# Kernel optimization log

Measured on AMD Instinct MI355X. Metric: run time of the kernel, lower is better.

The kernel has to match this reference:

```python
import jax, jax.numpy as jnp
import numpy as np

HEADS = 8
EPS = 1e-5


def setup_inputs() -> dict:
    key = jax.random.key(0)
    ks = jax.random.split(key, 4)
    B, S, N, C = 1, 192, 256, 256
    msa = jax.random.normal(ks[0], (B, S, N, C), dtype=jnp.float32)
    w_qkv = jax.random.normal(ks[1], (3 * C, C), dtype=jnp.float32) * 0.02
    b_qkv = jnp.zeros((3 * C,), dtype=jnp.float32)
    w_out = jax.random.normal(ks[2], (C, C), dtype=jnp.float32) * 0.02
    b_out = jnp.zeros((C,), dtype=jnp.float32)
    gamma = jnp.ones((C,), dtype=jnp.float32)
    beta = jnp.zeros((C,), dtype=jnp.float32)
    return {"msa": msa, "w_qkv": w_qkv, "b_qkv": b_qkv, "w_out": w_out,
            "b_out": b_out, "gamma": gamma, "beta": beta}


def reference(msa, w_qkv, b_qkv, w_out, b_out, gamma, beta):
    B, S, N, C = msa.shape
    H = HEADS
    D = C // H
    scale = D ** -0.5
    # column attention: attend over the S (MSA depth) axis per residue n
    msa_t = jnp.transpose(msa, (0, 2, 1, 3))                 # [B,N,S,C]
    qkv = msa_t @ w_qkv.T + b_qkv                             # [B,N,S,3C]
    qkv = qkv.reshape(B, N, S, 3, H, D)
    q, k, v = qkv[..., 0, :, :], qkv[..., 1, :, :], qkv[..., 2, :, :]  # [B,N,S,H,D]
    attn = jnp.einsum('bnshd,bnthd->bnhst', q, k) * scale     # [B,N,H,S,S]
    attn = jax.nn.softmax(attn, axis=-1)
    out = jnp.einsum('bnhst,bnthd->bnshd', attn, v).reshape(B, N, S, C)
    out = jnp.transpose(out, (0, 2, 1, 3))                    # [B,S,N,C]
    out = out @ w_out.T + b_out
    x = msa + out
    mu = jnp.mean(x, axis=-1, keepdims=True)
    var = jnp.mean(jnp.square(x - mu), axis=-1, keepdims=True)
    return (x - mu) * jax.lax.rsqrt(var + EPS) * gamma + beta
```

## Files before the change

### kernel.cpp

```cpp
#include <hip/hip_runtime.h>
#include <stdint.h>

#define S_DIM 192
#define N_DIM 256
#define C_DIM 256
#define H_DIM 8
#define D_DIM 32
#define TOK   (N_DIM * S_DIM)
#define QKV_STRIDE (N_DIM * H_DIM * S_DIM * D_DIM)

typedef float f32x4 __attribute__((ext_vector_type(4)));
typedef float f32x16 __attribute__((ext_vector_type(16)));
typedef short bf16x8 __attribute__((ext_vector_type(8)));

__device__ __forceinline__ unsigned short f2bf(float f) {
  union { float f; unsigned u; } v; v.f = f;
  unsigned r = v.u + 0x7FFFu + ((v.u >> 16) & 1u);
  return (unsigned short)(r >> 16);
}

__device__ __forceinline__ unsigned cvt_pk_bf16(float lo, float hi) {
  unsigned r;
  asm("v_cvt_pk_bf16_f32 %0, %1, %2" : "=v"(r) : "v"(lo), "v"(hi));
  return r;
}

__device__ __forceinline__ void gl2lds16(const void* g, void* l) {
  __builtin_amdgcn_global_load_lds(
      (const __attribute__((address_space(1))) unsigned int*)g,
      (__attribute__((address_space(3))) unsigned int*)l, 16, 0, 0);
}

__global__ __launch_bounds__(256) void k_prep(const float* __restrict__ msa,
                                              unsigned short* __restrict__ A,
                                              const float* __restrict__ wq,
                                              const float* __restrict__ wo,
                                              unsigned short* __restrict__ dq,
                                              unsigned short* __restrict__ do_) {
  int b = blockIdx.x;
  if (b < 12288) {
    int tid = b * 256 + threadIdx.x;
    int token = tid >> 6;
    int c4 = tid & 63;
    int n = token / S_DIM;
    int s = token - n * S_DIM;
    float4 v = *(const float4*)(msa + ((size_t)(s * N_DIM + n) << 8) + (c4 << 2));
    ushort4 o;
    o.x = f2bf(v.x); o.y = f2bf(v.y); o.z = f2bf(v.z); o.w = f2bf(v.w);
    *(ushort4*)(A + ((size_t)token << 8) + (c4 << 2)) = o;
  } else {
    int tid = (b - 12288) * 256 + threadIdx.x;
    const float* src; unsigned short* dst; int idx;
    if (tid < 49152) { src = wq; dst = dq; idx = tid; }
    else { src = wo; dst = do_; idx = tid - 49152; }
    float4 v = *(const float4*)(src + (size_t)idx * 4);
    ushort4 o;
    o.x = f2bf(v.x); o.y = f2bf(v.y); o.z = f2bf(v.z); o.w = f2bf(v.w);
    *(ushort4*)(dst + (size_t)idx * 4) = o;
  }
}

__global__ __launch_bounds__(256) void k_qkv(const unsigned short* __restrict__ A,
                                             const unsigned short* __restrict__ W,
                                             const float* __restrict__ bq,
                                             unsigned short* __restrict__ qkv) {
  __shared__ unsigned short As[128 * 64];
  __shared__ unsigned short Bs[128 * 64];
  const int tid = threadIdx.x;
  const int lane = tid & 63, wid = tid >> 6;
  const int l16 = lane & 15, lg = lane >> 4;
  const int wr = wid >> 1, wc = wid & 1;
  const int bm0 = blockIdx.x * 128;
  const int bn0 = blockIdx.y * 128;
  const int lrow = lane >> 3, lchunk = lane & 7;
  const int sw = ((lchunk ^ lrow) * 8);

  f32x4 acc[4][4] = {};

  for (int ks = 0; ks < 4; ks++) {
    const int k0 = ks * 64;
    __syncthreads();
#pragma unroll
    for (int q = 0; q < 4; q++) {
      int base_row = wid * 32 + q * 8;
      gl2lds16(A + (size_t)(bm0 + base_row + lrow) * 256 + k0 + sw, &As[base_row * 64]);
    }
#pragma unroll
    for (int q = 0; q < 4; q++) {
      int base_row = wid * 32 + q * 8;
      gl2lds16(W + (size_t)(bn0 + base_row + lrow) * 256 + k0 + sw, &Bs[base_row * 64]);
    }
    __syncthreads();
#pragma unroll
    for (int kk = 0; kk < 2; kk++) {
      const int xr = ((kk * 4 + lg) ^ (l16 & 7)) * 8;
      bf16x8 a[4], b[4];
#pragma unroll
      for (int m = 0; m < 4; m++)
        a[m] = *(const bf16x8*)&As[(wr * 64 + m * 16 + l16) * 64 + xr];
#pragma unroll
      for (int n2 = 0; n2 < 4; n2++)
        b[n2] = *(const bf16x8*)&Bs[(wc * 64 + n2 * 16 + l16) * 64 + xr];
      if (bn0 < 512) {
#pragma unroll
        for (int m = 0; m < 4; m++)
#pragma unroll
          for (int n2 = 0; n2 < 4; n2++)
            acc[m][n2] = __builtin_amdgcn_mfma_f32_16x16x32_bf16(b[n2], a[m], acc[m][n2], 0, 0, 0);
      } else {
#pragma unroll
        for (int m = 0; m < 4; m++)
#pragma unroll
          for (int n2 = 0; n2 < 4; n2++)
            acc[m][n2] = __builtin_amdgcn_mfma_f32_16x16x32_bf16(a[m], b[n2], acc[m][n2], 0, 0, 0);
      }
    }
  }

  const int t3 = bn0 >> 8;
  if (t3 < 2) {
#pragma unroll
    for (int n2 = 0; n2 < 4; n2++) {
      int j0 = bn0 + wc * 64 + n2 * 16 + lg * 4;
      float4 b4 = *(const float4*)&bq[j0];
      int c0 = j0 & 255;
      int h = c0 >> 5, d0 = c0 & 31;
#pragma unroll
      for (int m = 0; m < 4; m++) {
        int token = bm0 + wr * 64 + m * 16 + l16;
        int n = token / S_DIM;
        int s = token - n * S_DIM;
        ushort4 o;
        o.x = f2bf(acc[m][n2][0] + b4.x);
        o.y = f2bf(acc[m][n2][1] + b4.y);
        o.z = f2bf(acc[m][n2][2] + b4.z);
        o.w = f2bf(acc[m][n2][3] + b4.w);
        *(ushort4*)(qkv + (size_t)t3 * QKV_STRIDE +
                    ((size_t)((n * 8 + h) * 192 + s)) * 32 + d0) = o;
      }
    }
  } else {
#pragma unroll
    for (int n2 = 0; n2 < 4; n2++) {
      int j = bn0 + wc * 64 + n2 * 16 + l16;
      int hd = j - 512;
      int h = hd >> 5, d = hd & 31;
      float bias = bq[j];
#pragma unroll
      for (int m = 0; m < 4; m++) {
        int t0 = bm0 + wr * 64 + m * 16 + lg * 4;
        int n = t0 / S_DIM;
        int s0 = t0 - n * S_DIM;
        ushort4 o;
        o.x = f2bf(acc[m][n2][0] + bias);
        o.y = f2bf(acc[m][n2][1] + bias);
        o.z = f2bf(acc[m][n2][2] + bias);
        o.w = f2bf(acc[m][n2][3] + bias);
        *(ushort4*)(qkv + (size_t)2 * QKV_STRIDE + ((size_t)(n * 8 + h) * 32 + d) * 192 + s0) = o;
      }
    }
  }
}

__global__ __launch_bounds__(384) void k_attn2(const unsigned short* __restrict__ qkv,
                                               unsigned short* __restrict__ attn_out) {
  const int lane = threadIdx.x & 63;
  const int l32 = lane & 31;
  const int hi = lane >> 5;
  const int qt = threadIdx.x >> 6;
  const int nh = blockIdx.x;
  const int n = nh >> 3, h = nh & 7;
  const unsigned short* Qp = qkv + (size_t)nh * (192 * 32);
  const unsigned short* Kp = qkv + (size_t)QKV_STRIDE + (size_t)nh * (192 * 32);
  const unsigned short* Vt = qkv + (size_t)2 * QKV_STRIDE + (size_t)nh * (32 * 192);
  const int q0 = qt * 32;

  bf16x8 bq0 = *(const bf16x8*)(Qp + (q0 + l32) * 32 + hi * 8);
  bf16x8 bq1 = *(const bf16x8*)(Qp + (q0 + l32) * 32 + 16 + hi * 8);

  f32x16 accO = {};
  float m_run = -1e30f, l_run = 0.f;
  const float scale = 0.17677669529663687f;
  const float DEFER = 8.0f / 0.17677669529663687f;

  bf16x8 ka0 = *(const bf16x8*)(Kp + l32 * 32 + hi * 8);
  bf16x8 ka1 = *(const bf16x8*)(Kp + l32 * 32 + 16 + hi * 8);

  for (int t = 0; t < 6; t++) {
    bf16x8 kn0, kn1;
    if (t < 5) {
      kn0 = *(const bf16x8*)(Kp + ((t + 1) * 32 + l32) * 32 + hi * 8);
      kn1 = *(const bf16x8*)(Kp + ((t + 1) * 32 + l32) * 32 + 16 + hi * 8);
    }
    f32x16 sv = {};
    sv = __builtin_amdgcn_mfma_f32_32x32x16_bf16(ka0, bq0, sv, 0, 0, 0);
    sv = __builtin_amdgcn_mfma_f32_32x32x16_bf16(ka1, bq1, sv, 0, 0, 0);

    bf16x8 bv0 = *(const bf16x8*)(Vt + (size_t)l32 * 192 + t * 32 + hi * 8);
    bf16x8 bv1 = *(const bf16x8*)(Vt + (size_t)l32 * 192 + t * 32 + 16 + hi * 8);

    float tmx = sv[0];
#pragma unroll
    for (int r = 1; r < 16; r++) tmx = fmaxf(tmx, sv[r]);
    tmx = fmaxf(tmx, __shfl_xor(tmx, 32));

    bool need = tmx > m_run + DEFER;
    if (__ballot(need)) {
      float m_new = fmaxf(m_run, tmx);
      float corr = __expf((m_run - m_new) * scale);
      l_run *= corr;
#pragma unroll
      for (int r = 0; r < 16; r++) {
        int qr = (r & 3) + 8 * (r >> 2) + 4 * hi;
        accO[r] *= __shfl(corr, qr);
      }
      m_run = m_new;
    }

    float ssum = 0.f;
#pragma unroll
    for (int r = 0; r < 16; r++) {
      float p = __expf((sv[r] - m_run) * scale);
      sv[r] = p;
      ssum += p;
    }
    ssum += __shfl_xor(ssum, 32);
    l_run += ssum;

    unsigned pk[8];
#pragma unroll
    for (int g = 0; g < 4; g++) {
      pk[2 * g]     = cvt_pk_bf16(sv[4 * g],     sv[4 * g + 1]);
      pk[2 * g + 1] = cvt_pk_bf16(sv[4 * g + 2], sv[4 * g + 3]);
    }

#pragma unroll
    for (int kh = 0; kh < 2; kh++) {
      unsigned sa = hi ? pk[4 * kh]     : pk[4 * kh + 2];
      unsigned sb = hi ? pk[4 * kh + 1] : pk[4 * kh + 3];
      unsigned pa = __shfl_xor((int)sa, 32);
      unsigned pb = __shfl_xor((int)sb, 32);
      union { unsigned u[4]; bf16x8 v; } af;
      af.u[0] = hi ? pa : pk[4 * kh];
      af.u[1] = hi ? pb : pk[4 * kh + 1];
      af.u[2] = hi ? pk[4 * kh + 2] : pa;
      af.u[3] = hi ? pk[4 * kh + 3] : pb;
      accO = __builtin_amdgcn_mfma_f32_32x32x16_bf16(af.v, kh ? bv1 : bv0, accO, 0, 0, 0);
    }
    ka0 = kn0; ka1 = kn1;
  }

  float inv = 1.0f / l_run;
#pragma unroll
  for (int r = 0; r < 16; r++) {
    int qr = (r & 3) + 8 * (r >> 2) + 4 * hi;
    float v = accO[r] * __shfl(inv, qr);
    attn_out[((size_t)((q0 + qr) * 256 + n)) * 256 + h * 32 + l32] = f2bf(v);
  }
}

__global__ __launch_bounds__(256) void k_out(const unsigned short* __restrict__ Aat,
                                             const unsigned short* __restrict__ W,
                                             const float* __restrict__ bo,
                                             const float* __restrict__ msa,
                                             const float* __restrict__ gamma,
                                             const float* __restrict__ beta,
                                             float* __restrict__ out) {
  __shared__ unsigned short As[128 * 64];
  __shared__ unsigned short Bs[256 * 64];
  const int tid = threadIdx.x;
  const int lane = tid & 63, wid = tid >> 6;
  const int l16 = lane & 15, lg = lane >> 4;
  const int bm0 = blockIdx.x * 128;
  const int lrow = lane >> 3, lchunk = lane & 7;
  const int sw = ((lchunk ^ lrow) * 8);

  f32x4 acc[2][16] = {};

  for (int ks = 0; ks < 4; ks++) {
    const int k0 = ks * 64;
    __syncthreads();
#pragma unroll
    for (int q = 0; q < 4; q++) {
      int base_row = wid * 32 + q * 8;
      gl2lds16(Aat + (size_t)(bm0 + base_row + lrow) * 256 + k0 + sw, &As[base_row * 64]);
    }
#pragma unroll
    for (int q = 0; q < 8; q++) {
      int base_row = wid * 64 + q * 8;
      gl2lds16(W + (size_t)(base_row + lrow) * 256 + k0 + sw, &Bs[base_row * 64]);
    }
    __syncthreads();
#pragma unroll
    for (int kk = 0; kk < 2; kk++) {
      const int xr = ((kk * 4 + lg) ^ (l16 & 7)) * 8;
      bf16x8 a[2];
#pragma unroll
      for (int m = 0; m < 2; m++)
        a[m] = *(const bf16x8*)&As[(wid * 32 + m * 16 + l16) * 64 + xr];
#pragma unroll
      for (int c = 0; c < 16; c++) {
        bf16x8 b = *(const bf16x8*)&Bs[(c * 16 + l16) * 64 + xr];
#pragma unroll
        for (int m = 0; m < 2; m++)
          acc[m][c] = __builtin_amdgcn_mfma_f32_16x16x32_bf16(a[m], b, acc[m][c], 0, 0, 0);
      }
    }
  }

#pragma unroll
  for (int m = 0; m < 2; m++) {
#pragma unroll
    for (int c = 0; c < 16; c++) {
      int col = c * 16 + l16;
      float bias = bo[col];
#pragma unroll
      for (int i = 0; i < 4; i++) {
        int row = bm0 + wid * 32 + m * 16 + lg * 4 + i;
        acc[m][c][i] += bias + msa[(size_t)row * 256 + col];
      }
    }
#pragma unroll
    for (int i = 0; i < 4; i++) {
      float s1 = 0.f, s2 = 0.f;
#pragma unroll
      for (int c = 0; c < 16; c++) { float x = acc[m][c][i]; s1 += x; s2 += x * x; }
      s1 += __shfl_xor(s1, 1); s2 += __shfl_xor(s2, 1);
      s1 += __shfl_xor(s1, 2); s2 += __shfl_xor(s2, 2);
      s1 += __shfl_xor(s1, 4); s2 += __shfl_xor(s2, 4);
      s1 += __shfl_xor(s1, 8); s2 += __shfl_xor(s2, 8);
      float mu = s1 * (1.0f / 256.0f);
      float var = s2 * (1.0f / 256.0f) - mu * mu;
      float rstd = rsqrtf(var + 1e-5f);
      int row = bm0 + wid * 32 + m * 16 + lg * 4 + i;
#pragma unroll
      for (int c = 0; c < 16; c++) {
        int col = c * 16 + l16;
        float y = (acc[m][c][i] - mu) * rstd * gamma[col] + beta[col];
        out[(size_t)row * 256 + col] = y;
      }
    }
  }
}

extern "C" void kernel_launch(void* const* d_in, const int* in_sizes, int n_in,
                              void* d_out, int out_size, void* d_ws, size_t ws_size,
                              hipStream_t stream) {
  const float* msa   = (const float*)d_in[0];
  const float* w_qkv = (const float*)d_in[1];
  const float* b_qkv = (const float*)d_in[2];
  const float* w_out = (const float*)d_in[3];
  const float* b_out = (const float*)d_in[4];
  const float* gamma = (const float*)d_in[5];
  const float* beta  = (const float*)d_in[6];
  float* out = (float*)d_out;

  char* ws = (char*)d_ws;
  unsigned short* A      = (unsigned short*)(ws);
  unsigned short* qkvbuf = (unsigned short*)(ws + 25165824ull);
  unsigned short* wq_bf  = (unsigned short*)(ws + 4ull * 25165824ull);
  unsigned short* wo_bf  = (unsigned short*)(ws + 4ull * 25165824ull + 393216ull);

  k_prep<<<12544, 256, 0, stream>>>(msa, A, w_qkv, w_out, wq_bf, wo_bf);
  dim3 g2(384, 6);
  k_qkv<<<g2, 256, 0, stream>>>(A, wq_bf, b_qkv, qkvbuf);
  k_attn2<<<2048, 384, 0, stream>>>(qkvbuf, A);
  k_out<<<384, 256, 0, stream>>>(A, wo_bf, b_out, msa, gamma, beta, out);
}
```

Measured before the change: 127.0 us.

## Double-buffer LDS tiles in QKV projection GEMM to overlap loads with MFMA

```diff
diff --git a/kernel.cpp b/kernel.cpp
--- a/kernel.cpp
+++ b/kernel.cpp
@@ -6,7 +6,6 @@
 #define C_DIM 256
 #define H_DIM 8
 #define D_DIM 32
-#define TOK   (N_DIM * S_DIM)
 #define QKV_STRIDE (N_DIM * H_DIM * S_DIM * D_DIM)
 
 typedef float f32x4 __attribute__((ext_vector_type(4)));
@@ -64,8 +63,8 @@
                                              const unsigned short* __restrict__ W,
                                              const float* __restrict__ bq,
                                              unsigned short* __restrict__ qkv) {
-  __shared__ unsigned short As[128 * 64];
-  __shared__ unsigned short Bs[128 * 64];
+  __shared__ unsigned short As[2][128 * 64];
+  __shared__ unsigned short Bs[2][128 * 64];
   const int tid = threadIdx.x;
   const int lane = tid & 63, wid = tid >> 6;
   const int l16 = lane & 15, lg = lane >> 4;
@@ -77,30 +76,36 @@
 
   f32x4 acc[4][4] = {};
 
+#define STAGE_QKV(buf, k0)                                                     \
+  {                                                                            \
+    _Pragma("unroll")                                                          \
+    for (int q = 0; q < 4; q++) {                                              \
+      int base_row = wid * 32 + q * 8;                                         \
+      gl2lds16(A + (size_t)(bm0 + base_row + lrow) * 256 + (k0) + sw,          \
+               &As[buf][base_row * 64]);                                       \
+      gl2lds16(W + (size_t)(bn0 + base_row + lrow) * 256 + (k0) + sw,          \
+               &Bs[buf][base_row * 64]);                                       \
+    }                                                                          \
+  }
+
+  STAGE_QKV(0, 0);
+  asm volatile("s_waitcnt vmcnt(0)" ::: "memory");
+  __builtin_amdgcn_s_barrier();
+
+#pragma unroll
   for (int ks = 0; ks < 4; ks++) {
-    const int k0 = ks * 64;
-    __syncthreads();
-#pragma unroll
-    for (int q = 0; q < 4; q++) {
-      int base_row = wid * 32 + q * 8;
-      gl2lds16(A + (size_t)(bm0 + base_row + lrow) * 256 + k0 + sw, &As[base_row * 64]);
-    }
-#pragma unroll
-    for (int q = 0; q < 4; q++) {
-      int base_row = wid * 32 + q * 8;
-      gl2lds16(W + (size_t)(bn0 + base_row + lrow) * 256 + k0 + sw, &Bs[base_row * 64]);
-    }
-    __syncthreads();
+    const int cur = ks & 1;
+    if (ks < 3) STAGE_QKV(cur ^ 1, (ks + 1) * 64);
 #pragma unroll
     for (int kk = 0; kk < 2; kk++) {
       const int xr = ((kk * 4 + lg) ^ (l16 & 7)) * 8;
       bf16x8 a[4], b[4];
 #pragma unroll
       for (int m = 0; m < 4; m++)
-        a[m] = *(const bf16x8*)&As[(wr * 64 + m * 16 + l16) * 64 + xr];
+        a[m] = *(const bf16x8*)&As[cur][(wr * 64 + m * 16 + l16) * 64 + xr];
 #pragma unroll
       for (int n2 = 0; n2 < 4; n2++)
-        b[n2] = *(const bf16x8*)&Bs[(wc * 64 + n2 * 16 + l16) * 64 + xr];
+        b[n2] = *(const bf16x8*)&Bs[cur][(wc * 64 + n2 * 16 + l16) * 64 + xr];
       if (bn0 < 512) {
 #pragma unroll
         for (int m = 0; m < 4; m++)
@@ -115,7 +120,12 @@
             acc[m][n2] = __builtin_amdgcn_mfma_f32_16x16x32_bf16(a[m], b[n2], acc[m][n2], 0, 0, 0);
       }
     }
-  }
+    if (ks < 3) {
+      asm volatile("s_waitcnt vmcnt(0)" ::: "memory");
+      __builtin_amdgcn_s_barrier();
+    }
+  }
+#undef STAGE_QKV
 
   const int t3 = bn0 >> 8;
   if (t3 < 2) {
@@ -220,9 +230,9 @@
     float ssum = 0.f;
 #pragma unroll
     for (int r = 0; r < 16; r++) {
-      float p = __expf((sv[r] - m_run) * scale);
-      sv[r] = p;
-      ssum += p;
+      float p2 = __expf((sv[r] - m_run) * scale);
+      sv[r] = p2;
+      ssum += p2;
     }
     ssum += __shfl_xor(ssum, 32);
     l_run += ssum;
```

Measured after the change: 141.4 us. +11.4%, slower.
